# Kernel optimization log

Measured on AMD Instinct MI355X. Metric: run time of the kernel, lower is better.

Reference implementation:

```python
import jax, jax.numpy as jnp
import numpy as np


def _lin(x, w, b):
    return x @ w + b


def _fmv(x, w):
    # fused weighted mean/variance over the views axis (dim 2)
    mean = jnp.sum(x * w, axis=2, keepdims=True)
    var = jnp.sum(w * (x - mean) ** 2, axis=2, keepdims=True)
    return mean, var


def setup_inputs() -> dict:
    key = jax.random.key(0)
    ks = iter(jax.random.split(key, 40))
    R, S, V = 2048, 64, 8  # n_rays, n_samples, n_views

    def W(i, o):
        return jax.random.normal(next(ks), (i, o), jnp.float32) * (1.0 / np.sqrt(i))

    inp = {
        "rgb_feat": jax.random.normal(next(ks), (R, S, V, 35), jnp.float32),
        "neuray_feat": jax.random.normal(next(ks), (R, S, V, 32), jnp.float32),
        "ray_diff": jax.random.normal(next(ks), (R, S, V, 4), jnp.float32),
        "mask": (jax.random.uniform(next(ks), (R, S, V, 1)) > 0.1).astype(jnp.float32),
        "que_pts": jax.random.normal(next(ks), (R, S, 3), jnp.float32),
        "que_dir": jax.random.normal(next(ks), (R, S, 3), jnp.float32),
        # ray_dir_fc: Linear(4,16) ELU Linear(16,35) ELU
        "rd_w1": W(4, 16), "rd_b1": jnp.zeros(16, jnp.float32),
        "rd_w2": W(16, 35), "rd_b2": jnp.zeros(35, jnp.float32),
        # rgbfeat_fc: Linear(35,64) ReLU Linear(64,64)
        "rf_w1": W(35, 64), "rf_b1": jnp.zeros(64, jnp.float32),
        "rf_w2": W(64, 64), "rf_b2": jnp.zeros(64, jnp.float32),
        # neuray_fc: Linear(32,8) ELU Linear(8,1)
        "nr_w1": W(32, 8), "nr_b1": jnp.zeros(8, jnp.float32),
        "nr_w2": W(8, 1), "nr_b2": jnp.zeros(1, jnp.float32),
        # base_fc: Linear(207,64) ELU Linear(64,32) ELU
        "base_w1": W(207, 64), "base_b1": jnp.zeros(64, jnp.float32),
        "base_w2": W(64, 32), "base_b2": jnp.zeros(32, jnp.float32),
        # vis_fc: Linear(32,32) ELU Linear(32,33) ELU
        "vis_w1": W(32, 32), "vis_b1": jnp.zeros(32, jnp.float32),
        "vis_w2": W(32, 33), "vis_b2": jnp.zeros(33, jnp.float32),
        # vis_fc2: Linear(32,32) ELU Linear(32,1) Sigmoid
        "v2_w1": W(32, 32), "v2_b1": jnp.zeros(32, jnp.float32),
        "v2_w2": W(32, 1), "v2_b2": jnp.zeros(1, jnp.float32),
    }
    return inp


def reference(rgb_feat, neuray_feat, ray_diff, mask, que_pts, que_dir,
              rd_w1, rd_b1, rd_w2, rd_b2,
              rf_w1, rf_b1, rf_w2, rf_b2,
              nr_w1, nr_b1, nr_w2, nr_b2,
              base_w1, base_b1, base_w2, base_b2,
              vis_w1, vis_b1, vis_w2, vis_b2,
              v2_w1, v2_b1, v2_w2, v2_b2):
    elu = jax.nn.elu
    num_views = rgb_feat.shape[2]

    direction_feat = elu(_lin(elu(_lin(ray_diff, rd_w1, rd_b1)), rd_w2, rd_b2))
    rgb_feat_ = rgb_feat + direction_feat  # [R,S,V,35]

    rgb_feat_1 = _lin(jax.nn.relu(_lin(rgb_feat, rf_w1, rf_b1)), rf_w2, rf_b2)
    rgb_feat_max = jnp.max(rgb_feat_1, axis=2)  # [R,S,64]

    weight = mask / (jnp.sum(mask, axis=2, keepdims=True) + 1e-8)
    weight0 = jax.nn.sigmoid(_lin(elu(_lin(neuray_feat, nr_w1, nr_b1)), nr_w2, nr_b2))

    mean0, var0 = _fmv(rgb_feat_, weight0)
    mean1, var1 = _fmv(rgb_feat_, weight)
    globalfeat = jnp.concatenate([mean0, var0, mean1, var1], axis=-1)  # [R,S,1,140]

    gshape = globalfeat.shape[:2] + (num_views, globalfeat.shape[-1])
    x = jnp.concatenate([jnp.broadcast_to(globalfeat, gshape), rgb_feat_, neuray_feat], axis=-1)  # [R,S,V,207]
    x = elu(_lin(elu(_lin(x, base_w1, base_b1)), base_w2, base_b2))  # [R,S,V,32]

    x_vis = elu(_lin(elu(_lin(x * weight, vis_w1, vis_b1)), vis_w2, vis_b2))  # [R,S,V,33]
    x_res, vis = x_vis[..., :-1], x_vis[..., -1:]
    vis = jax.nn.sigmoid(vis) * mask
    x = x + x_res
    vis = jax.nn.sigmoid(_lin(elu(_lin(x * vis, v2_w1, v2_b1)), v2_w2, v2_b2)) * mask
    weight2 = vis / (jnp.sum(vis, axis=2, keepdims=True) + 1e-8)

    mean, var = _fmv(x, weight2)
    out = jnp.concatenate([mean[:, :, 0], var[:, :, 0]], axis=-1) + rgb_feat_max  # [R,S,64]
    return out
```

## Files before the change

kernel.cpp:

```cpp
#include <hip/hip_runtime.h>


#define NRS (2048*64)

__device__ __forceinline__ float eluf(float x){ return x > 0.f ? x : __expf(x)-1.f; }
__device__ __forceinline__ float sigmf(float x){ return 1.f/(1.f+__expf(-x)); }
__device__ __forceinline__ float sum8(float x){
    x += __shfl_xor(x, 1); x += __shfl_xor(x, 2); x += __shfl_xor(x, 4); return x;
}
__device__ __forceinline__ float max8(float x){
    x = fmaxf(x, __shfl_xor(x, 1)); x = fmaxf(x, __shfl_xor(x, 2)); x = fmaxf(x, __shfl_xor(x, 4)); return x;
}

__global__ __launch_bounds__(64, 2) void nerf_main(
    const float* __restrict__ g_rgb,  const float* __restrict__ g_nr,
    const float* __restrict__ g_rd,   const float* __restrict__ g_mask,
    const float* __restrict__ rd_w1,  const float* __restrict__ rd_b1,
    const float* __restrict__ rd_w2,  const float* __restrict__ rd_b2,
    const float* __restrict__ rf_w1,  const float* __restrict__ rf_b1,
    const float* __restrict__ rf_w2,  const float* __restrict__ rf_b2,
    const float* __restrict__ nr_w1,  const float* __restrict__ nr_b1,
    const float* __restrict__ nr_w2,  const float* __restrict__ nr_b2,
    const float* __restrict__ base_w1,const float* __restrict__ base_b1,
    const float* __restrict__ base_w2,const float* __restrict__ base_b2,
    const float* __restrict__ vis_w1, const float* __restrict__ vis_b1,
    const float* __restrict__ vis_w2, const float* __restrict__ vis_b2,
    const float* __restrict__ v2_w1,  const float* __restrict__ v2_b1,
    const float* __restrict__ v2_w2,  const float* __restrict__ v2_b2,
    float* __restrict__ out)
{
    __shared__ __align__(16) float g_lds[8*144];
    __shared__ float gc_lds  [8*65];
    __shared__ float gmax_lds[8*65];
    __shared__ float out_lds [512];

    const int lane = threadIdx.x;
    const int t    = lane >> 3;
    const int v    = lane & 7;
    const int pid  = blockIdx.x * 64 + lane;

    float rgb[35];
    #pragma unroll
    for (int k = 0; k < 35; ++k) rgb[k] = g_rgb[(size_t)pid*35 + k];
    float rdv[4];
    #pragma unroll
    for (int k = 0; k < 4; ++k) rdv[k] = g_rd[(size_t)pid*4 + k];
    float nrv[32];
    #pragma unroll
    for (int k = 0; k < 32; ++k) nrv[k] = g_nr[(size_t)pid*32 + k];
    const float mask = g_mask[pid];
    const float wt   = mask / (sum8(mask) + 1e-8f);

    float x64[64];
    {
        float acc[64];
        #pragma unroll
        for (int o = 0; o < 64; ++o) acc[o] = rf_b1[o];
        #pragma unroll 1
        for (int k = 0; k < 35; ++k) {
            const float xk = rgb[k];
            #pragma unroll
            for (int o = 0; o < 64; ++o) acc[o] = fmaf(xk, rf_w1[k*64 + o], acc[o]);
        }
        #pragma unroll
        for (int o = 0; o < 64; ++o) x64[o] = fmaxf(acc[o], 0.f);
    }

    {
        float h16[16];
        #pragma unroll
        for (int o = 0; o < 16; ++o) {
            float a = rd_b1[o];
            #pragma unroll
            for (int k = 0; k < 4; ++k) a = fmaf(rdv[k], rd_w1[k*16 + o], a);
            h16[o] = eluf(a);
        }
        #pragma unroll 1
        for (int o = 0; o < 35; ++o) {
            float a = rd_b2[o];
            #pragma unroll
            for (int k = 0; k < 16; ++k) a = fmaf(h16[k], rd_w2[k*35 + o], a);
            rgb[o] += eluf(a);
        }
    }

    {
        float acc[64];
        #pragma unroll
        for (int o = 0; o < 64; ++o) acc[o] = rf_b2[o];
        #pragma unroll 1
        for (int k = 0; k < 64; ++k) {
            const float xk = x64[k];
            #pragma unroll
            for (int o = 0; o < 64; ++o) acc[o] = fmaf(xk, rf_w2[k*64 + o], acc[o]);
        }
        #pragma unroll
        for (int o = 0; o < 64; ++o) {
            const float gm = max8(acc[o]);
            if (v == (o & 7)) gmax_lds[t*65 + o] = gm;
        }
    }

    float w0;
    {
        float h8[8];
        #pragma unroll
        for (int o = 0; o < 8; ++o) h8[o] = nr_b1[o];
        #pragma unroll 4
        for (int k = 0; k < 32; ++k) {
            const float xk = nrv[k];
            #pragma unroll
            for (int o = 0; o < 8; ++o) h8[o] = fmaf(xk, nr_w1[k*8 + o], h8[o]);
        }
        float a = nr_b2[0];
        #pragma unroll
        for (int k = 0; k < 8; ++k) a = fmaf(eluf(h8[k]), nr_w2[k], a);
        w0 = sigmf(a);
    }

    #pragma unroll 2
    for (int f = 0; f < 35; ++f) {
        const float a  = rgb[f];
        const float m0 = sum8(w0 * a);
        const float d0 = a - m0;
        const float v0 = sum8(w0 * d0 * d0);
        const float m1 = sum8(wt * a);
        const float d1 = a - m1;
        const float v1 = sum8(wt * d1 * d1);
        if (v == (f & 7)) {
            g_lds[t*144 + f]       = m0;
            g_lds[t*144 + 35 + f]  = v0;
            g_lds[t*144 + 70 + f]  = m1;
            g_lds[t*144 + 105 + f] = v1;
        }
    }
    __syncthreads();

    {
        float ga[8];
        #pragma unroll
        for (int q = 0; q < 8; ++q) ga[q] = 0.f;
        #pragma unroll 1
        for (int i = 0; i < 140; i += 4) {
            float w_[4];
            #pragma unroll
            for (int j = 0; j < 4; ++j) w_[j] = base_w1[(i + j)*64 + lane];
            #pragma unroll
            for (int q = 0; q < 8; ++q) {
                const float4 gv = *reinterpret_cast<const float4*>(&g_lds[q*144 + i]);
                ga[q] = fmaf(gv.x, w_[0], ga[q]);
                ga[q] = fmaf(gv.y, w_[1], ga[q]);
                ga[q] = fmaf(gv.z, w_[2], ga[q]);
                ga[q] = fmaf(gv.w, w_[3], ga[q]);
            }
        }
        #pragma unroll
        for (int q = 0; q < 8; ++q) gc_lds[q*65 + lane] = ga[q];
    }
    __syncthreads();

    {
        float acc[64];
        #pragma unroll
        for (int o = 0; o < 64; ++o) acc[o] = base_b1[o] + gc_lds[t*65 + o];
        #pragma unroll 1
        for (int k = 0; k < 35; ++k) {
            const float xk = rgb[k];
            #pragma unroll
            for (int o = 0; o < 64; ++o) acc[o] = fmaf(xk, base_w1[(140+k)*64 + o], acc[o]);
        }
        #pragma unroll 1
        for (int k = 0; k < 32; ++k) {
            const float xk = nrv[k];
            #pragma unroll
            for (int o = 0; o < 64; ++o) acc[o] = fmaf(xk, base_w1[(175+k)*64 + o], acc[o]);
        }
        #pragma unroll
        for (int o = 0; o < 64; ++o) x64[o] = eluf(acc[o]);
    }

    float x2[32];
    {
        #pragma unroll
        for (int o = 0; o < 32; ++o) x2[o] = base_b2[o];
        #pragma unroll 2
        for (int k = 0; k < 64; ++k) {
            const float xk = x64[k];
            #pragma unroll
            for (int o = 0; o < 32; ++o) x2[o] = fmaf(xk, base_w2[k*32 + o], x2[o]);
        }
        #pragma unroll
        for (int o = 0; o < 32; ++o) x2[o] = eluf(x2[o]);
    }

    float hv[32];
    {
        float acc[32];
        #pragma unroll
        for (int o = 0; o < 32; ++o) acc[o] = 0.f;
        #pragma unroll 2
        for (int k = 0; k < 32; ++k) {
            const float xk = x2[k];
            #pragma unroll
            for (int o = 0; o < 32; ++o) acc[o] = fmaf(xk, vis_w1[k*32 + o], acc[o]);
        }
        #pragma unroll
        for (int o = 0; o < 32; ++o) hv[o] = eluf(fmaf(acc[o], wt, vis_b1[o]));
    }
    float vis1;
    {
        float acc[32];
        #pragma unroll
        for (int o = 0; o < 32; ++o) acc[o] = vis_b2[o];
        float a2 = vis_b2[32];
        #pragma unroll 2
        for (int k = 0; k < 32; ++k) {
            const float hk = hv[k];
            #pragma unroll
            for (int o = 0; o < 32; ++o) acc[o] = fmaf(hk, vis_w2[k*33 + o], acc[o]);
            a2 = fmaf(hk, vis_w2[k*33 + 32], a2);
        }
        #pragma unroll
        for (int o = 0; o < 32; ++o) x2[o] += eluf(acc[o]);
        vis1 = sigmf(eluf(a2)) * mask;
    }

    float vis2;
    {
        float acc[32];
        #pragma unroll
        for (int o = 0; o < 32; ++o) acc[o] = 0.f;
        #pragma unroll 2
        for (int k = 0; k < 32; ++k) {
            const float xk = x2[k];
            #pragma unroll
            for (int o = 0; o < 32; ++o) acc[o] = fmaf(xk, v2_w1[k*32 + o], acc[o]);
        }
        float a = v2_b2[0];
        #pragma unroll
        for (int k = 0; k < 32; ++k) a = fmaf(eluf(fmaf(acc[k], vis1, v2_b1[k])), v2_w2[k], a);
        vis2 = sigmf(a) * mask;
    }

    {
        const float w2 = vis2 / (sum8(vis2) + 1e-8f);
        #pragma unroll 2
        for (int c = 0; c < 32; ++c) {
            const float xv = x2[c];
            const float m  = sum8(w2 * xv);
            const float d  = xv - m;
            const float va = sum8(w2 * d * d);
            if (v == (c & 7)) {
                out_lds[t*64 + c]      = m  + gmax_lds[t*65 + c];
                out_lds[t*64 + 32 + c] = va + gmax_lds[t*65 + 32 + c];
            }
        }
    }
    __syncthreads();

    const size_t ob = (size_t)blockIdx.x * 512;
    #pragma unroll
    for (int j = 0; j < 8; ++j)
        out[ob + j*64 + lane] = out_lds[j*64 + lane];
}

extern "C" void kernel_launch(void* const* d_in, const int* in_sizes, int n_in,
                              void* d_out, int out_size, void* d_ws, size_t ws_size,
                              hipStream_t stream) {
    const float* g_rgb   = (const float*)d_in[0];
    const float* g_nr    = (const float*)d_in[1];
    const float* g_rd    = (const float*)d_in[2];
    const float* g_mask  = (const float*)d_in[3];
    const float* rd_w1   = (const float*)d_in[6];
    const float* rd_b1   = (const float*)d_in[7];
    const float* rd_w2   = (const float*)d_in[8];
    const float* rd_b2   = (const float*)d_in[9];
    const float* rf_w1   = (const float*)d_in[10];
    const float* rf_b1   = (const float*)d_in[11];
    const float* rf_w2   = (const float*)d_in[12];
    const float* rf_b2   = (const float*)d_in[13];
    const float* nr_w1   = (const float*)d_in[14];
    const float* nr_b1   = (const float*)d_in[15];
    const float* nr_w2   = (const float*)d_in[16];
    const float* nr_b2   = (const float*)d_in[17];
    const float* base_w1 = (const float*)d_in[18];
    const float* base_b1 = (const float*)d_in[19];
    const float* base_w2 = (const float*)d_in[20];
    const float* base_b2 = (const float*)d_in[21];
    const float* vis_w1  = (const float*)d_in[22];
    const float* vis_b1  = (const float*)d_in[23];
    const float* vis_w2  = (const float*)d_in[24];
    const float* vis_b2  = (const float*)d_in[25];
    const float* v2_w1   = (const float*)d_in[26];
    const float* v2_b1   = (const float*)d_in[27];
    const float* v2_w2   = (const float*)d_in[28];
    const float* v2_b2   = (const float*)d_in[29];
    float* out = (float*)d_out;

    hipLaunchKernelGGL(nerf_main, dim3(NRS / 8), dim3(64), 0, stream,
        g_rgb, g_nr, g_rd, g_mask,
        rd_w1, rd_b1, rd_w2, rd_b2,
        rf_w1, rf_b1, rf_w2, rf_b2,
        nr_w1, nr_b1, nr_w2, nr_b2,
        base_w1, base_b1, base_w2, base_b2,
        vis_w1, vis_b1, vis_w2, vis_b2,
        v2_w1, v2_b1, v2_w2, v2_b2,
        out);
}
```

Baseline: 1.305 ms.

## Remap MLP to output-per-lane with LDS-staged activations and pre-transposed weights

The kernel is restructured so each lane owns one output channel across 16 points (2 rays × 8 views) instead of one point with all channels in registers. Activations are staged in LDS in a k4-interleaved layout, and weights are pre-transposed into float4-friendly order by a separate prep kernel writing to workspace. This cuts register pressure and replaces per-element scalar weight loads and shuffle reductions with vectorized loads and register FMAs. The cost is an extra launch, heavy LDS traffic, and no __syncthreads between stages, which is only safe because each block is a single wavefront.

Result: slower. 1.632 ms (+25.0%).

```diff
diff --git a/kernel.cpp b/kernel.cpp
--- a/kernel.cpp
+++ b/kernel.cpp
@@ -1,267 +1,414 @@
 #include <hip/hip_runtime.h>
 
 
-#define NRS (2048*64)
+#define NRS  (2048*64)
+#define NBLK (NRS/2)
+
+#define X_RGB 0
+#define X_NR  756
+#define X_ACT 1428
+#define X_H16 2772
+#define X_RD  3108
+#define X_G   3172
+#define X_X2  3460
+#define X_HV  4132
+#define X_GMX 4804
+#define SC_MASK 4932
+#define SC_WT   4948
+#define SC_W0   4964
+#define SC_V1   4980
+#define SC_V2   4996
+#define LDS_TOT 5012
+
+#define WT_RF1 0
+#define WT_RF2 2304
+#define WT_RD2 6400
+#define WT_B1G 7424
+#define WT_B1V 16384
+#define WT_B2  20736
+#define WT_V1  22784
+#define WT_V2  23808
+#define WT_U1  24832
+#define WT_TOT 25856
 
 __device__ __forceinline__ float eluf(float x){ return x > 0.f ? x : __expf(x)-1.f; }
 __device__ __forceinline__ float sigmf(float x){ return 1.f/(1.f+__expf(-x)); }
-__device__ __forceinline__ float sum8(float x){
-    x += __shfl_xor(x, 1); x += __shfl_xor(x, 2); x += __shfl_xor(x, 4); return x;
-}
-__device__ __forceinline__ float max8(float x){
-    x = fmaxf(x, __shfl_xor(x, 1)); x = fmaxf(x, __shfl_xor(x, 2)); x = fmaxf(x, __shfl_xor(x, 4)); return x;
+
+__global__ __launch_bounds__(256) void transpose_w(
+    const float* __restrict__ rf_w1, const float* __restrict__ rf_w2,
+    const float* __restrict__ rd_w2, const float* __restrict__ base_w1,
+    const float* __restrict__ base_w2, const float* __restrict__ vis_w1,
+    const float* __restrict__ vis_w2, const float* __restrict__ v2_w1,
+    float* __restrict__ ws)
+{
+    int i = blockIdx.x * 256 + threadIdx.x;
+    if (i < WT_RF2) {
+        int k4 = i >> 8, r = i & 255, o = r >> 2, j = r & 3, k = k4*4 + j;
+        ws[i] = (k < 35) ? rf_w1[k*64 + o] : 0.f;
+    } else if (i < WT_RD2) {
+        int j2 = i - WT_RF2;
+        int k4 = j2 >> 8, r = j2 & 255, o = r >> 2, j = r & 3, k = k4*4 + j;
+        ws[i] = rf_w2[k*64 + o];
+    } else if (i < WT_B1G) {
+        int j2 = i - WT_RD2;
+        int k4 = j2 >> 8, r = j2 & 255, o = r >> 2, j = r & 3, k = k4*4 + j;
+        ws[i] = (o < 35) ? rd_w2[k*35 + o] : 0.f;
+    } else if (i < WT_B1V) {
+        int j2 = i - WT_B1G;
+        int k4 = j2 >> 8, r = j2 & 255, o = r >> 2, j = r & 3, k = k4*4 + j;
+        ws[i] = base_w1[k*64 + o];
+    } else if (i < WT_B2) {
+        int j2 = i - WT_B1V;
+        int k4 = j2 >> 8, r = j2 & 255, o = r >> 2, j = r & 3;
+        float v = 0.f;
+        if (k4 < 9) { int k = k4*4 + j; if (k < 35) v = base_w1[(140 + k)*64 + o]; }
+        else        { int k = (k4 - 9)*4 + j;       v = base_w1[(175 + k)*64 + o]; }
+        ws[i] = v;
+    } else if (i < WT_V1) {
+        int j2 = i - WT_B2;
+        int k4 = j2 >> 7, r = j2 & 127, o = r >> 2, j = r & 3, k = k4*4 + j;
+        ws[i] = base_w2[k*32 + o];
+    } else if (i < WT_V2) {
+        int j2 = i - WT_V1;
+        int k4 = j2 >> 7, r = j2 & 127, o = r >> 2, j = r & 3, k = k4*4 + j;
+        ws[i] = vis_w1[k*32 + o];
+    } else if (i < WT_U1) {
+        int j2 = i - WT_V2;
+        int k4 = j2 >> 7, r = j2 & 127, o = r >> 2, j = r & 3, k = k4*4 + j;
+        ws[i] = vis_w2[k*33 + o];
+    } else if (i < WT_TOT) {
+        int j2 = i - WT_U1;
+        int k4 = j2 >> 7, r = j2 & 127, o = r >> 2, j = r & 3, k = k4*4 + j;
+        ws[i] = v2_w1[k*32 + o];
+    }
 }
 
 __global__ __launch_bounds__(64, 2) void nerf_main(
     const float* __restrict__ g_rgb,  const float* __restrict__ g_nr,
     const float* __restrict__ g_rd,   const float* __restrict__ g_mask,
     const float* __restrict__ rd_w1,  const float* __restrict__ rd_b1,
-    const float* __restrict__ rd_w2,  const float* __restrict__ rd_b2,
-    const float* __restrict__ rf_w1,  const float* __restrict__ rf_b1,
-    const float* __restrict__ rf_w2,  const float* __restrict__ rf_b2,
+    const float* __restrict__ rd_b2,
+    const float* __restrict__ rf_b1,  const float* __restrict__ rf_b2,
     const float* __restrict__ nr_w1,  const float* __restrict__ nr_b1,
     const float* __restrict__ nr_w2,  const float* __restrict__ nr_b2,
-    const float* __restrict__ base_w1,const float* __restrict__ base_b1,
-    const float* __restrict__ base_w2,const float* __restrict__ base_b2,
-    const float* __restrict__ vis_w1, const float* __restrict__ vis_b1,
-    const float* __restrict__ vis_w2, const float* __restrict__ vis_b2,
-    const float* __restrict__ v2_w1,  const float* __restrict__ v2_b1,
-    const float* __restrict__ v2_w2,  const float* __restrict__ v2_b2,
+    const float* __restrict__ base_b1,const float* __restrict__ base_b2,
+    const float* __restrict__ vis_b1, const float* __restrict__ vis_w2,
+    const float* __restrict__ vis_b2,
+    const float* __restrict__ v2_b1,  const float* __restrict__ v2_w2,
+    const float* __restrict__ v2_b2,
+    const float* __restrict__ W,
     float* __restrict__ out)
 {
-    __shared__ __align__(16) float g_lds[8*144];
-    __shared__ float gc_lds  [8*65];
-    __shared__ float gmax_lds[8*65];
-    __shared__ float out_lds [512];
-
+    __shared__ __align__(16) float Sf[LDS_TOT];
     const int lane = threadIdx.x;
-    const int t    = lane >> 3;
-    const int v    = lane & 7;
-    const int pid  = blockIdx.x * 64 + lane;
-
-    float rgb[35];
-    #pragma unroll
-    for (int k = 0; k < 35; ++k) rgb[k] = g_rgb[(size_t)pid*35 + k];
-    float rdv[4];
-    #pragma unroll
-    for (int k = 0; k < 4; ++k) rdv[k] = g_rd[(size_t)pid*4 + k];
-    float nrv[32];
-    #pragma unroll
-    for (int k = 0; k < 32; ++k) nrv[k] = g_nr[(size_t)pid*32 + k];
-    const float mask = g_mask[pid];
-    const float wt   = mask / (sum8(mask) + 1e-8f);
-
-    float x64[64];
-    {
-        float acc[64];
-        #pragma unroll
-        for (int o = 0; o < 64; ++o) acc[o] = rf_b1[o];
-        #pragma unroll 1
-        for (int k = 0; k < 35; ++k) {
-            const float xk = rgb[k];
+    const size_t b = blockIdx.x;
+
+    {
+        const float* src = g_rgb + b*560;
+        #pragma unroll
+        for (int it = 0; it < 9; ++it) {
+            int idx = it*64 + lane;
+            if (idx < 560) {
+                int p = idx / 35, k = idx - p*35;
+                Sf[X_RGB + (k>>2)*84 + p*4 + (k&3)] = src[idx];
+            }
+        }
+        if (lane < 16) Sf[X_RGB + 8*84 + lane*4 + 3] = 0.f;
+        const float* srcn = g_nr + b*512;
+        #pragma unroll
+        for (int it = 0; it < 8; ++it) {
+            int idx = it*64 + lane;
+            int p = idx >> 5, k = idx & 31;
+            Sf[X_NR + (k>>2)*84 + p*4 + (k&3)] = srcn[idx];
+        }
+        Sf[X_RD + (lane&3)*16 + (lane>>2)] = g_rd[b*64 + lane];
+        if (lane < 16) {
+            float m = g_mask[b*16 + lane];
+            float s = m;
+            s += __shfl_xor(s,1); s += __shfl_xor(s,2); s += __shfl_xor(s,4);
+            Sf[SC_MASK + lane] = m;
+            Sf[SC_WT   + lane] = m / (s + 1e-8f);
+        }
+    }
+
+#define STEP16(ACC, XBASE, W4) { \
+        _Pragma("unroll") \
+        for (int p = 0; p < 16; ++p) { \
+            const float4 xv = *reinterpret_cast<const float4*>(&Sf[(XBASE) + p*4]); \
+            ACC[p] = fmaf(xv.x, (W4).x, ACC[p]); \
+            ACC[p] = fmaf(xv.y, (W4).y, ACC[p]); \
+            ACC[p] = fmaf(xv.z, (W4).z, ACC[p]); \
+            ACC[p] = fmaf(xv.w, (W4).w, ACC[p]); \
+        } }
+
+    {
+        float acc[16];
+        const float bb = rf_b1[lane];
+        #pragma unroll
+        for (int p = 0; p < 16; ++p) acc[p] = bb;
+        #pragma unroll 1
+        for (int k4 = 0; k4 < 9; ++k4) {
+            const float4 w4 = *reinterpret_cast<const float4*>(&W[WT_RF1 + k4*256 + lane*4]);
+            STEP16(acc, X_RGB + k4*84, w4);
+        }
+        #pragma unroll
+        for (int p = 0; p < 16; ++p)
+            Sf[X_ACT + (lane>>2)*84 + p*4 + (lane&3)] = fmaxf(acc[p], 0.f);
+    }
+
+    {
+        float acc[16];
+        const float bb = rf_b2[lane];
+        #pragma unroll
+        for (int p = 0; p < 16; ++p) acc[p] = bb;
+        #pragma unroll 1
+        for (int k4 = 0; k4 < 16; ++k4) {
+            const float4 w4 = *reinterpret_cast<const float4*>(&W[WT_RF2 + k4*256 + lane*4]);
+            STEP16(acc, X_ACT + k4*84, w4);
+        }
+        float g0 = acc[0], g1 = acc[8];
+        #pragma unroll
+        for (int p = 1; p < 8; ++p) { g0 = fmaxf(g0, acc[p]); g1 = fmaxf(g1, acc[8+p]); }
+        Sf[X_GMX + lane]      = g0;
+        Sf[X_GMX + 64 + lane] = g1;
+    }
+
+    {
+        const int p = lane >> 2, og4 = lane & 3;
+        float4 h = *reinterpret_cast<const float4*>(&rd_b1[og4*4]);
+        #pragma unroll
+        for (int k = 0; k < 4; ++k) {
+            const float xk = Sf[X_RD + k*16 + p];
+            const float4 w4 = *reinterpret_cast<const float4*>(&rd_w1[k*16 + og4*4]);
+            h.x = fmaf(xk, w4.x, h.x); h.y = fmaf(xk, w4.y, h.y);
+            h.z = fmaf(xk, w4.z, h.z); h.w = fmaf(xk, w4.w, h.w);
+        }
+        h.x = eluf(h.x); h.y = eluf(h.y); h.z = eluf(h.z); h.w = eluf(h.w);
+        *reinterpret_cast<float4*>(&Sf[X_H16 + og4*84 + p*4]) = h;
+    }
+
+    if (lane < 35) {
+        float acc[16];
+        const float bb = rd_b2[lane];
+        #pragma unroll
+        for (int p = 0; p < 16; ++p) acc[p] = bb;
+        #pragma unroll 1
+        for (int k4 = 0; k4 < 4; ++k4) {
+            const float4 w4 = *reinterpret_cast<const float4*>(&W[WT_RD2 + k4*256 + lane*4]);
+            STEP16(acc, X_H16 + k4*84, w4);
+        }
+        #pragma unroll
+        for (int p = 0; p < 16; ++p) {
+            const int idx = X_RGB + (lane>>2)*84 + p*4 + (lane&3);
+            Sf[idx] += eluf(acc[p]);
+        }
+    }
+
+    {
+        const int p = lane >> 2, og = lane & 3;
+        float h0 = nr_b1[og*2], h1 = nr_b1[og*2 + 1];
+        #pragma unroll
+        for (int k = 0; k < 32; ++k) {
+            const float xk = Sf[X_NR + (k>>2)*84 + p*4 + (k&3)];
+            const float2 w2 = *reinterpret_cast<const float2*>(&nr_w1[k*8 + og*2]);
+            h0 = fmaf(xk, w2.x, h0); h1 = fmaf(xk, w2.y, h1);
+        }
+        const float2 v2 = *reinterpret_cast<const float2*>(&nr_w2[og*2]);
+        float part = eluf(h0)*v2.x + eluf(h1)*v2.y;
+        part += __shfl_xor(part, 1); part += __shfl_xor(part, 2);
+        if (og == 0) Sf[SC_W0 + p] = sigmf(part + nr_b2[0]);
+    }
+
+    if (lane < 35) {
+        float xf[16], w0v[16], wtv[16];
+        #pragma unroll
+        for (int p = 0; p < 16; ++p) {
+            xf[p]  = Sf[X_RGB + (lane>>2)*84 + p*4 + (lane&3)];
+            w0v[p] = Sf[SC_W0 + p];
+            wtv[p] = Sf[SC_WT + p];
+        }
+        #pragma unroll
+        for (int rs = 0; rs < 2; ++rs) {
+            const int o8 = rs*8;
+            float m0 = 0.f, m1 = 0.f;
             #pragma unroll
-            for (int o = 0; o < 64; ++o) acc[o] = fmaf(xk, rf_w1[k*64 + o], acc[o]);
-        }
-        #pragma unroll
-        for (int o = 0; o < 64; ++o) x64[o] = fmaxf(acc[o], 0.f);
-    }
-
-    {
-        float h16[16];
-        #pragma unroll
-        for (int o = 0; o < 16; ++o) {
-            float a = rd_b1[o];
+            for (int p = 0; p < 8; ++p) {
+                m0 = fmaf(w0v[o8+p], xf[o8+p], m0);
+                m1 = fmaf(wtv[o8+p], xf[o8+p], m1);
+            }
+            float v0 = 0.f, v1 = 0.f;
             #pragma unroll
-            for (int k = 0; k < 4; ++k) a = fmaf(rdv[k], rd_w1[k*16 + o], a);
-            h16[o] = eluf(a);
-        }
-        #pragma unroll 1
-        for (int o = 0; o < 35; ++o) {
-            float a = rd_b2[o];
-            #pragma unroll
-            for (int k = 0; k < 16; ++k) a = fmaf(h16[k], rd_w2[k*35 + o], a);
-            rgb[o] += eluf(a);
-        }
-    }
-
-    {
-        float acc[64];
-        #pragma unroll
-        for (int o = 0; o < 64; ++o) acc[o] = rf_b2[o];
-        #pragma unroll 1
-        for (int k = 0; k < 64; ++k) {
-            const float xk = x64[k];
-            #pragma unroll
-            for (int o = 0; o < 64; ++o) acc[o] = fmaf(xk, rf_w2[k*64 + o], acc[o]);
-        }
-        #pragma unroll
-        for (int o = 0; o < 64; ++o) {
-            const float gm = max8(acc[o]);
-            if (v == (o & 7)) gmax_lds[t*65 + o] = gm;
-        }
-    }
-
-    float w0;
-    {
-        float h8[8];
-        #pragma unroll
-        for (int o = 0; o < 8; ++o) h8[o] = nr_b1[o];
-        #pragma unroll 4
-        for (int k = 0; k < 32; ++k) {
-            const float xk = nrv[k];
-            #pragma unroll
-            for (int o = 0; o < 8; ++o) h8[o] = fmaf(xk, nr_w1[k*8 + o], h8[o]);
-        }
-        float a = nr_b2[0];
-        #pragma unroll
-        for (int k = 0; k < 8; ++k) a = fmaf(eluf(h8[k]), nr_w2[k], a);
-        w0 = sigmf(a);
-    }
-
-    #pragma unroll 2
-    for (int f = 0; f < 35; ++f) {
-        const float a  = rgb[f];
-        const float m0 = sum8(w0 * a);
-        const float d0 = a - m0;
-        const float v0 = sum8(w0 * d0 * d0);
-        const float m1 = sum8(wt * a);
-        const float d1 = a - m1;
-        const float v1 = sum8(wt * d1 * d1);
-        if (v == (f & 7)) {
-            g_lds[t*144 + f]       = m0;
-            g_lds[t*144 + 35 + f]  = v0;
-            g_lds[t*144 + 70 + f]  = m1;
-            g_lds[t*144 + 105 + f] = v1;
-        }
-    }
-    __syncthreads();
-
-    {
-        float ga[8];
-        #pragma unroll
-        for (int q = 0; q < 8; ++q) ga[q] = 0.f;
-        #pragma unroll 1
-        for (int i = 0; i < 140; i += 4) {
-            float w_[4];
-            #pragma unroll
-            for (int j = 0; j < 4; ++j) w_[j] = base_w1[(i + j)*64 + lane];
-            #pragma unroll
-            for (int q = 0; q < 8; ++q) {
-                const float4 gv = *reinterpret_cast<const float4*>(&g_lds[q*144 + i]);
-                ga[q] = fmaf(gv.x, w_[0], ga[q]);
-                ga[q] = fmaf(gv.y, w_[1], ga[q]);
-                ga[q] = fmaf(gv.z, w_[2], ga[q]);
-                ga[q] = fmaf(gv.w, w_[3], ga[q]);
+            for (int p = 0; p < 8; ++p) {
+                const float d0 = xf[o8+p] - m0, d1 = xf[o8+p] - m1;
+                v0 = fmaf(w0v[o8+p]*d0, d0, v0);
+                v1 = fmaf(wtv[o8+p]*d1, d1, v1);
             }
-        }
-        #pragma unroll
-        for (int q = 0; q < 8; ++q) gc_lds[q*65 + lane] = ga[q];
-    }
-    __syncthreads();
-
-    {
-        float acc[64];
-        #pragma unroll
-        for (int o = 0; o < 64; ++o) acc[o] = base_b1[o] + gc_lds[t*65 + o];
-        #pragma unroll 1
-        for (int k = 0; k < 35; ++k) {
-            const float xk = rgb[k];
-            #pragma unroll
-            for (int o = 0; o < 64; ++o) acc[o] = fmaf(xk, base_w1[(140+k)*64 + o], acc[o]);
-        }
-        #pragma unroll 1
-        for (int k = 0; k < 32; ++k) {
-            const float xk = nrv[k];
-            #pragma unroll
-            for (int o = 0; o < 64; ++o) acc[o] = fmaf(xk, base_w1[(175+k)*64 + o], acc[o]);
-        }
-        #pragma unroll
-        for (int o = 0; o < 64; ++o) x64[o] = eluf(acc[o]);
-    }
-
-    float x2[32];
-    {
-        #pragma unroll
-        for (int o = 0; o < 32; ++o) x2[o] = base_b2[o];
-        #pragma unroll 2
-        for (int k = 0; k < 64; ++k) {
-            const float xk = x64[k];
-            #pragma unroll
-            for (int o = 0; o < 32; ++o) x2[o] = fmaf(xk, base_w2[k*32 + o], x2[o]);
-        }
-        #pragma unroll
-        for (int o = 0; o < 32; ++o) x2[o] = eluf(x2[o]);
-    }
-
-    float hv[32];
-    {
-        float acc[32];
-        #pragma unroll
-        for (int o = 0; o < 32; ++o) acc[o] = 0.f;
-        #pragma unroll 2
-        for (int k = 0; k < 32; ++k) {
-            const float xk = x2[k];
-            #pragma unroll
-            for (int o = 0; o < 32; ++o) acc[o] = fmaf(xk, vis_w1[k*32 + o], acc[o]);
-        }
-        #pragma unroll
-        for (int o = 0; o < 32; ++o) hv[o] = eluf(fmaf(acc[o], wt, vis_b1[o]));
-    }
-    float vis1;
-    {
-        float acc[32];
-        #pragma unroll
-        for (int o = 0; o < 32; ++o) acc[o] = vis_b2[o];
-        float a2 = vis_b2[32];
-        #pragma unroll 2
-        for (int k = 0; k < 32; ++k) {
-            const float hk = hv[k];
-            #pragma unroll
-            for (int o = 0; o < 32; ++o) acc[o] = fmaf(hk, vis_w2[k*33 + o], acc[o]);
-            a2 = fmaf(hk, vis_w2[k*33 + 32], a2);
-        }
-        #pragma unroll
-        for (int o = 0; o < 32; ++o) x2[o] += eluf(acc[o]);
-        vis1 = sigmf(eluf(a2)) * mask;
-    }
-
-    float vis2;
-    {
-        float acc[32];
-        #pragma unroll
-        for (int o = 0; o < 32; ++o) acc[o] = 0.f;
-        #pragma unroll 2
-        for (int k = 0; k < 32; ++k) {
-            const float xk = x2[k];
-            #pragma unroll
-            for (int o = 0; o < 32; ++o) acc[o] = fmaf(xk, v2_w1[k*32 + o], acc[o]);
-        }
-        float a = v2_b2[0];
-        #pragma unroll
-        for (int k = 0; k < 32; ++k) a = fmaf(eluf(fmaf(acc[k], vis1, v2_b1[k])), v2_w2[k], a);
-        vis2 = sigmf(a) * mask;
-    }
-
-    {
-        const float w2 = vis2 / (sum8(vis2) + 1e-8f);
-        #pragma unroll 2
-        for (int c = 0; c < 32; ++c) {
-            const float xv = x2[c];
-            const float m  = sum8(w2 * xv);
-            const float d  = xv - m;
-            const float va = sum8(w2 * d * d);
-            if (v == (c & 7)) {
-                out_lds[t*64 + c]      = m  + gmax_lds[t*65 + c];
-                out_lds[t*64 + 32 + c] = va + gmax_lds[t*65 + 32 + c];
-            }
-        }
-    }
-    __syncthreads();
-
-    const size_t ob = (size_t)blockIdx.x * 512;
-    #pragma unroll
-    for (int j = 0; j < 8; ++j)
-        out[ob + j*64 + lane] = out_lds[j*64 + lane];
+            Sf[X_G + rs*144 + lane]       = m0;
+            Sf[X_G + rs*144 + 35 + lane]  = v0;
+            Sf[X_G + rs*144 + 70 + lane]  = m1;
+            Sf[X_G + rs*144 + 105 + lane] = v1;
+        }
+    }
+
+    float gc0 = 0.f, gc1 = 0.f;
+    {
+        #pragma unroll 1
+        for (int i4 = 0; i4 < 35; ++i4) {
+            const float4 w4 = *reinterpret_cast<const float4*>(&W[WT_B1G + i4*256 + lane*4]);
+            const float4 ga = *reinterpret_cast<const float4*>(&Sf[X_G + i4*4]);
+            const float4 gb = *reinterpret_cast<const float4*>(&Sf[X_G + 144 + i4*4]);
+            gc0 = fmaf(ga.x,w4.x, fmaf(ga.y,w4.y, fmaf(ga.z,w4.z, fmaf(ga.w,w4.w, gc0))));
+            gc1 = fmaf(gb.x,w4.x, fmaf(gb.y,w4.y, fmaf(gb.z,w4.z, fmaf(gb.w,w4.w, gc1))));
+        }
+    }
+
+    {
+        float acc[16];
+        const float bb = base_b1[lane];
+        #pragma unroll
+        for (int p = 0; p < 16; ++p) acc[p] = bb + (p < 8 ? gc0 : gc1);
+        #pragma unroll 1
+        for (int k4 = 0; k4 < 9; ++k4) {
+            const float4 w4 = *reinterpret_cast<const float4*>(&W[WT_B1V + k4*256 + lane*4]);
+            STEP16(acc, X_RGB + k4*84, w4);
+        }
+        #pragma unroll 1
+        for (int k4 = 0; k4 < 8; ++k4) {
+            const float4 w4 = *reinterpret_cast<const float4*>(&W[WT_B1V + (9+k4)*256 + lane*4]);
+            STEP16(acc, X_NR + k4*84, w4);
+        }
+        #pragma unroll
+        for (int p = 0; p < 16; ++p)
+            Sf[X_ACT + (lane>>2)*84 + p*4 + (lane&3)] = eluf(acc[p]);
+    }
+
+#define STEP8(ACC, XBASE, W4, H) { \
+        _Pragma("unroll") \
+        for (int p = 0; p < 8; ++p) { \
+            const float4 xv = *reinterpret_cast<const float4*>(&Sf[(XBASE) + ((H)*8 + p)*4]); \
+            ACC[p] = fmaf(xv.x, (W4).x, ACC[p]); \
+            ACC[p] = fmaf(xv.y, (W4).y, ACC[p]); \
+            ACC[p] = fmaf(xv.z, (W4).z, ACC[p]); \
+            ACC[p] = fmaf(xv.w, (W4).w, ACC[p]); \
+        } }
+
+    const int o32 = lane & 31, hh = lane >> 5;
+
+    {
+        float acc[8];
+        const float bb = base_b2[o32];
+        #pragma unroll
+        for (int p = 0; p < 8; ++p) acc[p] = bb;
+        #pragma unroll 1
+        for (int k4 = 0; k4 < 16; ++k4) {
+            const float4 w4 = *reinterpret_cast<const float4*>(&W[WT_B2 + k4*128 + o32*4]);
+            STEP8(acc, X_ACT + k4*84, w4, hh);
+        }
+        #pragma unroll
+        for (int p = 0; p < 8; ++p)
+            Sf[X_X2 + (o32>>2)*84 + (hh*8+p)*4 + (o32&3)] = eluf(acc[p]);
+    }
+
+    {
+        float acc[8];
+        #pragma unroll
+        for (int p = 0; p < 8; ++p) acc[p] = 0.f;
+        #pragma unroll 1
+        for (int k4 = 0; k4 < 8; ++k4) {
+            const float4 w4 = *reinterpret_cast<const float4*>(&W[WT_V1 + k4*128 + o32*4]);
+            STEP8(acc, X_X2 + k4*84, w4, hh);
+        }
+        const float bb = vis_b1[o32];
+        #pragma unroll
+        for (int p = 0; p < 8; ++p)
+            Sf[X_HV + (o32>>2)*84 + (hh*8+p)*4 + (o32&3)] =
+                eluf(fmaf(acc[p], Sf[SC_WT + hh*8 + p], bb));
+    }
+
+    {
+        float acc[8];
+        const float bb = vis_b2[o32];
+        #pragma unroll
+        for (int p = 0; p < 8; ++p) acc[p] = bb;
+        #pragma unroll 1
+        for (int k4 = 0; k4 < 8; ++k4) {
+            const float4 w4 = *reinterpret_cast<const float4*>(&W[WT_V2 + k4*128 + o32*4]);
+            STEP8(acc, X_HV + k4*84, w4, hh);
+        }
+        #pragma unroll
+        for (int p = 0; p < 8; ++p) {
+            const int idx = X_X2 + (o32>>2)*84 + (hh*8+p)*4 + (o32&3);
+            Sf[idx] += eluf(acc[p]);
+        }
+    }
+
+    {
+        const int p = lane >> 2, q = lane & 3;
+        float a = 0.f;
+        #pragma unroll
+        for (int j = 0; j < 8; ++j) {
+            const int k = q*8 + j;
+            a = fmaf(Sf[X_HV + (k>>2)*84 + p*4 + (k&3)], vis_w2[k*33 + 32], a);
+        }
+        a += __shfl_xor(a, 1); a += __shfl_xor(a, 2);
+        if (q == 0)
+            Sf[SC_V1 + p] = sigmf(eluf(a + vis_b2[32])) * Sf[SC_MASK + p];
+    }
+
+    {
+        float acc[8];
+        #pragma unroll
+        for (int p = 0; p < 8; ++p) acc[p] = 0.f;
+        #pragma unroll 1
+        for (int k4 = 0; k4 < 8; ++k4) {
+            const float4 w4 = *reinterpret_cast<const float4*>(&W[WT_U1 + k4*128 + o32*4]);
+            STEP8(acc, X_X2 + k4*84, w4, hh);
+        }
+        const float bb = v2_b1[o32];
+        #pragma unroll
+        for (int p = 0; p < 8; ++p)
+            Sf[X_HV + (o32>>2)*84 + (hh*8+p)*4 + (o32&3)] =
+                eluf(fmaf(acc[p], Sf[SC_V1 + hh*8 + p], bb));
+    }
+
+    {
+        const int p = lane >> 2, q = lane & 3;
+        float a = 0.f;
+        #pragma unroll
+        for (int j = 0; j < 8; ++j) {
+            const int k = q*8 + j;
+            a = fmaf(Sf[X_HV + (k>>2)*84 + p*4 + (k&3)], v2_w2[k], a);
+        }
+        a += __shfl_xor(a, 1); a += __shfl_xor(a, 2);
+        if (q == 0)
+            Sf[SC_V2 + p] = sigmf(a + v2_b2[0]) * Sf[SC_MASK + p];
+    }
+
+    {
+        const int rs = lane >> 5, c = lane & 31;
+        float vv[8], xs[8];
+        #pragma unroll
+        for (int p = 0; p < 8; ++p) {
+            vv[p] = Sf[SC_V2 + rs*8 + p];
+            xs[p] = Sf[X_X2 + (c>>2)*84 + (rs*8+p)*4 + (c&3)];
+        }
+        float Vs = 0.f;
+        #pragma unroll
+        for (int p = 0; p < 8; ++p) Vs += vv[p];
+        const float inv = 1.f / (Vs + 1e-8f);
+        float m = 0.f;
+        #pragma unroll
+        for (int p = 0; p < 8; ++p) m = fmaf(vv[p]*inv, xs[p], m);
+        float var = 0.f;
+        #pragma unroll
+        for (int p = 0; p < 8; ++p) {
+            const float d = xs[p] - m;
+            var = fmaf(vv[p]*inv*d, d, var);
+        }
+        const size_t ob = b*128 + (size_t)rs*64;
+        out[ob + c]      = m   + Sf[X_GMX + rs*64 + c];
+        out[ob + 32 + c] = var + Sf[X_GMX + rs*64 + 32 + c];
+    }
 }
 
 extern "C" void kernel_launch(void* const* d_in, const int* in_sizes, int n_in,
@@ -295,15 +442,19 @@
     const float* v2_b1   = (const float*)d_in[27];
     const float* v2_w2   = (const float*)d_in[28];
     const float* v2_b2   = (const float*)d_in[29];
+    float* ws  = (float*)d_ws;
     float* out = (float*)d_out;
 
-    hipLaunchKernelGGL(nerf_main, dim3(NRS / 8), dim3(64), 0, stream,
+    hipLaunchKernelGGL(transpose_w, dim3((WT_TOT + 255)/256), dim3(256), 0, stream,
+                       rf_w1, rf_w2, rd_w2, base_w1, base_w2, vis_w1, vis_w2, v2_w1, ws);
+
+    hipLaunchKernelGGL(nerf_main, dim3(NBLK), dim3(64), 0, stream,
         g_rgb, g_nr, g_rd, g_mask,
-        rd_w1, rd_b1, rd_w2, rd_b2,
-        rf_w1, rf_b1, rf_w2, rf_b2,
+        rd_w1, rd_b1, rd_b2,
+        rf_b1, rf_b2,
         nr_w1, nr_b1, nr_w2, nr_b2,
-        base_w1, base_b1, base_w2, base_b2,
-        vis_w1, vis_b1, vis_w2, vis_b2,
-        v2_w1, v2_b1, v2_w2, v2_b2,
-        out);
+        base_b1, base_b2,
+        vis_b1, vis_w2, vis_b2,
+        v2_b1, v2_w2, v2_b2,
+        ws, out);
 }
```
